# Kernel tuning notes

Hardware: AMD Instinct MI355X
Metric: run time of the kernel (lower is better)

## Reference

```python
import jax, jax.numpy as jnp
import numpy as np

N_EMBD = 1024
N_HEAD = 16
DIM_HEAD = N_EMBD // N_HEAD
# Source code divides scores by scale = dim_head**-0.5, i.e. multiplies by sqrt(dim_head).
INV_SCALE = 1.0 / (DIM_HEAD ** -0.5)


def setup_inputs() -> dict:
    key = jax.random.key(0)
    k1, k2, k3 = jax.random.split(key, 3)
    x = jax.random.normal(k1, (4, 2048, N_EMBD), dtype=jnp.float32)
    # Linear(n_embd, 3*n_embd, bias=False): y = x @ W_qkv  (W stored as [C, 3C])
    W_qkv = jax.random.normal(k2, (N_EMBD, 3 * N_EMBD), dtype=jnp.float32) * (N_EMBD ** -0.5)
    W_proj = jax.random.normal(k3, (N_EMBD, N_EMBD), dtype=jnp.float32) * (N_EMBD ** -0.5)
    return {"x": x, "W_qkv": W_qkv, "W_proj": W_proj}


def reference(x, W_qkv, W_proj):
    B, T, C = x.shape
    qkv = jnp.einsum('btc,cd->btd', x, W_qkv)  # [B,T,3C]
    q, k, v = jnp.split(qkv, 3, axis=-1)
    # [B,T,C] -> [B,H,T,Dh]
    def to_heads(t):
        return t.reshape(B, T, N_HEAD, DIM_HEAD).transpose(0, 2, 1, 3)
    q, k, v = to_heads(q), to_heads(k), to_heads(v)
    scores = jnp.einsum('bhqd,bhkd->bhqk', q, k) * INV_SCALE  # faithful to /scale bug
    causal = jnp.tril(jnp.ones((T, T), dtype=bool))
    scores = jnp.where(causal[None, None], scores, -jnp.inf)
    attn = jax.nn.softmax(scores, axis=-1)
    y = jnp.einsum('bhqk,bhkd->bhqd', attn, v)  # [B,H,T,Dh]
    y = y.transpose(0, 2, 1, 3).reshape(B, T, C)
    return jnp.einsum('btc,cd->btd', y, W_proj)
```

## Files before the change

### kernel.cpp

```cpp
#include <hip/hip_runtime.h>
#include <stdint.h>

typedef unsigned short ushort_t;
typedef __attribute__((ext_vector_type(8))) short short8;
typedef __attribute__((ext_vector_type(8))) _Float16 half8;
typedef __attribute__((ext_vector_type(4))) float f32x4;
typedef __attribute__((ext_vector_type(4))) unsigned short us4;

#define AS1 __attribute__((address_space(1)))
#define AS3 __attribute__((address_space(3)))

#if __has_builtin(__builtin_amdgcn_exp2f)
#define EXP2(x) __builtin_amdgcn_exp2f(x)
#else
#define EXP2(x) exp2f(x)
#endif

#define SC 11.541560327111707f

__device__ __forceinline__ ushort_t f2h(float f) {
  _Float16 h = (_Float16)f;
  return __builtin_bit_cast(unsigned short, h);
}

__device__ __forceinline__ void gload16(const void* g, void* l) {
  __builtin_amdgcn_global_load_lds((AS1 const void*)g, (AS3 void*)l, 16, 0, 0);
}

__device__ __forceinline__ f32x4 mfma16(short8 a, short8 b, f32x4 c) {
  return __builtin_amdgcn_mfma_f32_16x16x32_f16(
      __builtin_bit_cast(half8, a), __builtin_bit_cast(half8, b), c, 0, 0, 0);
}

__global__ __launch_bounds__(256) void cast_f32_f16(const float4* __restrict__ in,
                                                    us4* __restrict__ out, int n4) {
  int i = blockIdx.x * 256 + threadIdx.x;
  int stride = gridDim.x * 256;
  for (; i < n4; i += stride) {
    float4 v = in[i];
    us4 o;
    o[0] = f2h(v.x); o[1] = f2h(v.y); o[2] = f2h(v.z); o[3] = f2h(v.w);
    out[i] = o;
  }
}

__global__ __launch_bounds__(256) void tcast(const float* __restrict__ in,
                                             ushort_t* __restrict__ out, int R, int C) {
  __shared__ __align__(16) float lt[32][33];
  const int r0 = blockIdx.y * 32, c0 = blockIdx.x * 32;
  const int i = threadIdx.x;
  const int lr = i >> 3, lc = (i & 7) * 4;
  float4 v = *(const float4*)(in + (size_t)(r0 + lr) * C + c0 + lc);
  lt[lr][lc + 0] = v.x; lt[lr][lc + 1] = v.y; lt[lr][lc + 2] = v.z; lt[lr][lc + 3] = v.w;
  __syncthreads();
  const int oc = i >> 3;
  const int orr = (i & 7) * 4;
  us4 o;
#pragma unroll
  for (int jj = 0; jj < 4; ++jj) o[jj] = f2h(lt[orr + jj][oc]);
  *(us4*)(out + (size_t)(c0 + oc) * R + r0 + orr) = o;
}

template<int MODE>
__global__ __launch_bounds__(256) void gemm128(
    const ushort_t* __restrict__ A, const ushort_t* __restrict__ Bt, int K, int N,
    ushort_t* __restrict__ qo, ushort_t* __restrict__ ko, ushort_t* __restrict__ vo,
    float* __restrict__ outp)
{
  __shared__ __align__(16) unsigned char lds[32768];
  const int tid = threadIdx.x;
  const int lane = tid & 63, w = tid >> 6;
  const int ln = lane & 15, gq = lane >> 4;
  const int wr = w >> 1, wc = w & 1;
  const int m0 = blockIdx.y * 128, n0 = blockIdx.x * 128;
  const size_t ldb = (size_t)K * 2;
  const unsigned char* ab = (const unsigned char*)A + (size_t)m0 * ldb;
  const unsigned char* bb = (const unsigned char*)Bt + (size_t)n0 * ldb;
  f32x4 acc[4][4] = {};
  const int nkt = K >> 6;
  for (int kb = 0; kb < nkt; ++kb) {
    const unsigned char* abk = ab + kb * 128;
    const unsigned char* bbk = bb + kb * 128;
#pragma unroll
    for (int e = 0; e < 4; ++e) {
      unsigned o = e * 4096 + tid * 16;
      unsigned r = o >> 7;
      unsigned c = (o & 127) ^ ((r & 7) << 4);
      gload16(abk + (size_t)r * ldb + c, lds + o);
      gload16(bbk + (size_t)r * ldb + c, lds + 16384 + o);
    }
    __syncthreads();
    short8 af[4][2], bf8[4][2];
#pragma unroll
    for (int mi = 0; mi < 4; ++mi) {
      unsigned row = wr * 64 + mi * 16 + ln;
      unsigned c0 = (gq * 16) ^ ((row & 7) << 4);
      af[mi][0] = *(const short8*)(lds + row * 128 + c0);
      af[mi][1] = *(const short8*)(lds + row * 128 + (c0 ^ 64));
    }
#pragma unroll
    for (int ni = 0; ni < 4; ++ni) {
      unsigned row = wc * 64 + ni * 16 + ln;
      unsigned c0 = (gq * 16) ^ ((row & 7) << 4);
      bf8[ni][0] = *(const short8*)(lds + 16384 + row * 128 + c0);
      bf8[ni][1] = *(const short8*)(lds + 16384 + row * 128 + (c0 ^ 64));
    }
#pragma unroll
    for (int mi = 0; mi < 4; ++mi)
#pragma unroll
      for (int ni = 0; ni < 4; ++ni) {
        acc[mi][ni] = mfma16(af[mi][0], bf8[ni][0], acc[mi][ni]);
        acc[mi][ni] = mfma16(af[mi][1], bf8[ni][1], acc[mi][ni]);
      }
    __syncthreads();
  }
  if (MODE == 0) {
#pragma unroll
    for (int mi = 0; mi < 4; ++mi)
#pragma unroll
      for (int ni = 0; ni < 4; ++ni) {
        int feat = n0 + wc * 64 + ni * 16 + ln;
        int sec = feat >> 10, cc = feat & 1023;
        int hh = cc >> 6, dd = cc & 63;
        int tokbase = m0 + wr * 64 + mi * 16 + gq * 4;
        int bh = (tokbase >> 11) * 16 + hh;
        int tloc = tokbase & 2047;
        if (sec == 2) {
          us4 pk;
#pragma unroll
          for (int j = 0; j < 4; ++j) pk[j] = f2h(acc[mi][ni][j]);
          *(us4*)(vo + ((size_t)bh * 64 + dd) * 2048 + tloc) = pk;
        } else {
          ushort_t* dst = (sec == 0) ? qo : ko;
#pragma unroll
          for (int j = 0; j < 4; ++j) {
            size_t off = ((size_t)bh * 2048 + tloc + j) * 64 + dd;
            dst[off] = f2h(acc[mi][ni][j]);
          }
        }
      }
  } else {
#pragma unroll
    for (int mi = 0; mi < 4; ++mi)
#pragma unroll
      for (int ni = 0; ni < 4; ++ni)
#pragma unroll
        for (int j = 0; j < 4; ++j) {
          int token = m0 + wr * 64 + mi * 16 + gq * 4 + j;
          int feat  = n0 + wc * 64 + ni * 16 + ln;
          outp[(size_t)token * N + feat] = acc[mi][ni][j];
        }
  }
}

__global__ __launch_bounds__(256) void attn_kernel(const ushort_t* __restrict__ qg,
                                                   const ushort_t* __restrict__ kg,
                                                   const ushort_t* __restrict__ vtg,
                                                   ushort_t* __restrict__ yg) {
  __shared__ __align__(16) unsigned char lds[40960];
  const int n = blockIdx.x;
  const int xcd = n & 7, loc = n >> 3;
  const int bh = xcd * 8 + (loc >> 4);
  const int pair = loc & 15;
  const int tid = threadIdx.x;
  const int lane = tid & 63, w = tid >> 6;
  const int ln = lane & 15, gq = lane >> 4;

  const unsigned char* kbase = (const unsigned char*)kg + (size_t)bh * 2048 * 128;
  const unsigned char* vbase = (const unsigned char*)vtg + (size_t)bh * 64 * 4096;
  const ushort_t* qg_bh = qg + (size_t)bh * 2048 * 64;
  const unsigned pw = 32768 + w * 2048;

  auto stage = [&](int buf, int t) {
    const unsigned char* kt = kbase + (size_t)t * 8192;
    const unsigned char* vt = vbase + t * 128;
#pragma unroll
    for (int e = 0; e < 2; ++e) {
      unsigned o = e * 4096 + tid * 16;
      unsigned r = o >> 7;
      unsigned c = (o & 127) ^ ((r & 7) << 4);
      gload16(kt + r * 128 + c, lds + buf * 8192 + o);
      gload16(vt + (size_t)r * 4096 + c, lds + 16384 + buf * 8192 + o);
    }
  };

  int cur = 0;
  for (int ph = 0; ph < 2; ++ph) {
    const int qt = (ph == 0) ? pair : 31 - pair;
    const int q0 = qt * 64;
    const int nt = qt + 1;

    const ushort_t* qrow = qg_bh + (size_t)(q0 + w * 16 + ln) * 64;
    short8 qa0 = *(const short8*)(qrow + gq * 8);
    short8 qa1 = *(const short8*)(qrow + 32 + gq * 8);

    f32x4 yacc[4] = {};
    float mrow = -3e38f, lrow = 0.f;

    stage(cur, 0);
    __syncthreads();

    for (int t = 0; t < nt; ++t) {
      if (t + 1 < nt) stage(cur ^ 1, t + 1);
      const unsigned kb_ = cur * 8192;
      const unsigned vb_ = 16384 + cur * 8192;
      f32x4 s[4];
      __builtin_amdgcn_s_setprio(1);
#pragma unroll
      for (int f = 0; f < 4; ++f) {
        unsigned row = f * 16 + ln;
        unsigned c0 = (gq * 16) ^ ((row & 7) << 4);
        short8 k0 = *(const short8*)(lds + kb_ + row * 128 + c0);
        short8 k1 = *(const short8*)(lds + kb_ + row * 128 + (c0 ^ 64));
        f32x4 z = {0.f, 0.f, 0.f, 0.f};
        z = mfma16(k0, qa0, z);
        s[f] = mfma16(k1, qa1, z);
      }
      __builtin_amdgcn_s_setprio(0);
      if (t == nt - 1) {
        int qloc = w * 16 + ln;
#pragma unroll
        for (int f = 0; f < 4; ++f) {
          int kvb = f * 16 + gq * 4;
#pragma unroll
          for (int j = 0; j < 4; ++j)
            if (kvb + j > qloc) s[f][j] = -3e38f;
        }
      }
      {
        float rm = s[0][0];
#pragma unroll
        for (int f = 0; f < 4; ++f)
#pragma unroll
          for (int j = 0; j < 4; ++j) rm = fmaxf(rm, s[f][j]);
        rm = fmaxf(rm, __shfl_xor(rm, 16));
        rm = fmaxf(rm, __shfl_xor(rm, 32));
        if (__any((rm - mrow) * SC > 8.0f)) {
          float mnew = fmaxf(mrow, rm);
          float alpha = EXP2((mrow - mnew) * SC);
          lrow *= alpha;
          mrow = mnew;
#pragma unroll
          for (int j = 0; j < 4; ++j) {
            float aj = __shfl(alpha, gq * 4 + j);
#pragma unroll
            for (int df = 0; df < 4; ++df) yacc[df][j] *= aj;
          }
        }
        float msc = mrow * SC;
        float rs = 0.f;
#pragma unroll
        for (int f = 0; f < 4; ++f)
#pragma unroll
          for (int j = 0; j < 4; ++j) {
            float p = EXP2(__builtin_fmaf(s[f][j], SC, -msc));
            s[f][j] = p;
            rs += p;
          }
        rs += __shfl_xor(rs, 16);
        rs += __shfl_xor(rs, 32);
        lrow += rs;
      }
#pragma unroll
      for (int f = 0; f < 4; ++f) {
        us4 pk;
#pragma unroll
        for (int j = 0; j < 4; ++j) pk[j] = f2h(s[f][j]);
        unsigned addr = (pw + ln * 128 + (f * 16 + gq * 4) * 2) ^ ((ln & 7) << 4);
        *(us4*)(lds + addr) = pk;
      }
      __builtin_amdgcn_s_setprio(1);
#pragma unroll
      for (int st = 0; st < 2; ++st) {
        unsigned pc = (st * 64 + gq * 16) ^ ((ln & 7) << 4);
        short8 pa = *(const short8*)(lds + pw + ln * 128 + pc);
#pragma unroll
        for (int df = 0; df < 4; ++df) {
          unsigned row = df * 16 + ln;
          unsigned c0 = (st * 64 + gq * 16) ^ ((row & 7) << 4);
          short8 vb = *(const short8*)(lds + vb_ + row * 128 + c0);
          yacc[df] = mfma16(pa, vb, yacc[df]);
        }
      }
      __builtin_amdgcn_s_setprio(0);
      __syncthreads();
      cur ^= 1;
    }

#pragma unroll
    for (int j = 0; j < 4; ++j) {
      float lj = __shfl(lrow, gq * 4 + j);
      float rl = 1.0f / lj;
      int tq = q0 + w * 16 + gq * 4 + j;
#pragma unroll
      for (int df = 0; df < 4; ++df) {
        int col = (bh & 15) * 64 + df * 16 + ln;
        size_t off = ((size_t)(bh >> 4) * 2048 + tq) * 1024 + col;
        yg[off] = f2h(yacc[df][j] * rl);
      }
    }
  }
}

extern "C" void kernel_launch(void* const* d_in, const int* in_sizes, int n_in,
                              void* d_out, int out_size, void* d_ws, size_t ws_size,
                              hipStream_t stream) {
  (void)in_sizes; (void)n_in; (void)out_size; (void)ws_size;
  const float* x     = (const float*)d_in[0];
  const float* wqkv  = (const float*)d_in[1];
  const float* wproj = (const float*)d_in[2];
  float* out = (float*)d_out;
  char* ws = (char*)d_ws;
  ushort_t* xb   = (ushort_t*)(ws);
  ushort_t* wqkt = (ushort_t*)(ws + 16777216);
  ushort_t* wpt  = (ushort_t*)(ws + 23068672);
  ushort_t* qb_  = (ushort_t*)(ws + 25165824);
  ushort_t* kb_  = (ushort_t*)(ws + 41943040);
  ushort_t* vt   = (ushort_t*)(ws + 75497472);
  ushort_t* yb   = xb;

  cast_f32_f16<<<2048, 256, 0, stream>>>((const float4*)x, (us4*)xb, 2097152);
  tcast<<<dim3(96, 32), 256, 0, stream>>>(wqkv, wqkt, 1024, 3072);
  tcast<<<dim3(32, 32), 256, 0, stream>>>(wproj, wpt, 1024, 1024);
  gemm128<0><<<dim3(24, 64), 256, 0, stream>>>(xb, wqkt, 1024, 3072, qb_, kb_, vt, nullptr);
  attn_kernel<<<1024, 256, 0, stream>>>(qb_, kb_, vt, yb);
  gemm128<1><<<dim3(8, 64), 256, 0, stream>>>(yb, wpt, 1024, 1024, nullptr, nullptr, nullptr, out);
}
```

Before: 186.7 us.

## Load K and V fragments directly from global memory instead of LDS staging

Removes the double-buffered asynchronous LDS staging of K and V tiles and the per-iteration block barrier. Each wave now reads its K and V^T MFMA fragments straight from global memory into registers, and LDS shrinks to the per-wave P scratch. This cuts LDS footprint and synchronization, which may raise occupancy. The cost is that all four waves load the same K/V data redundantly through L1/L2 and global latency is no longer hidden by prefetch.

```diff
diff --git a/kernel.cpp b/kernel.cpp
--- a/kernel.cpp
+++ b/kernel.cpp
@@ -157,7 +157,7 @@
                                                    const ushort_t* __restrict__ kg,
                                                    const ushort_t* __restrict__ vtg,
                                                    ushort_t* __restrict__ yg) {
-  __shared__ __align__(16) unsigned char lds[40960];
+  __shared__ __align__(16) unsigned char lds[8192];
   const int n = blockIdx.x;
   const int xcd = n & 7, loc = n >> 3;
   const int bh = xcd * 8 + (loc >> 4);
@@ -166,25 +166,11 @@
   const int lane = tid & 63, w = tid >> 6;
   const int ln = lane & 15, gq = lane >> 4;
 
-  const unsigned char* kbase = (const unsigned char*)kg + (size_t)bh * 2048 * 128;
-  const unsigned char* vbase = (const unsigned char*)vtg + (size_t)bh * 64 * 4096;
+  const ushort_t* kg_bh = kg + (size_t)bh * 2048 * 64;
+  const ushort_t* vt_bh = vtg + (size_t)bh * 64 * 2048;
   const ushort_t* qg_bh = qg + (size_t)bh * 2048 * 64;
-  const unsigned pw = 32768 + w * 2048;
-
-  auto stage = [&](int buf, int t) {
-    const unsigned char* kt = kbase + (size_t)t * 8192;
-    const unsigned char* vt = vbase + t * 128;
-#pragma unroll
-    for (int e = 0; e < 2; ++e) {
-      unsigned o = e * 4096 + tid * 16;
-      unsigned r = o >> 7;
-      unsigned c = (o & 127) ^ ((r & 7) << 4);
-      gload16(kt + r * 128 + c, lds + buf * 8192 + o);
-      gload16(vt + (size_t)r * 4096 + c, lds + 16384 + buf * 8192 + o);
-    }
-  };
-
-  int cur = 0;
+  const unsigned pw = w * 2048;
+
   for (int ph = 0; ph < 2; ++ph) {
     const int qt = (ph == 0) ? pair : 31 - pair;
     const int q0 = qt * 64;
@@ -197,24 +183,22 @@
     f32x4 yacc[4] = {};
     float mrow = -3e38f, lrow = 0.f;
 
-    stage(cur, 0);
-    __syncthreads();
-
     for (int t = 0; t < nt; ++t) {
-      if (t + 1 < nt) stage(cur ^ 1, t + 1);
-      const unsigned kb_ = cur * 8192;
-      const unsigned vb_ = 16384 + cur * 8192;
+      const ushort_t* kt_g = kg_bh + (size_t)t * 64 * 64;
+      short8 kf0[4], kf1[4];
+#pragma unroll
+      for (int f = 0; f < 4; ++f) {
+        const ushort_t* kr = kt_g + (unsigned)(f * 16 + ln) * 64 + gq * 8;
+        kf0[f] = *(const short8*)kr;
+        kf1[f] = *(const short8*)(kr + 32);
+      }
       f32x4 s[4];
       __builtin_amdgcn_s_setprio(1);
 #pragma unroll
       for (int f = 0; f < 4; ++f) {
-        unsigned row = f * 16 + ln;
-        unsigned c0 = (gq * 16) ^ ((row & 7) << 4);
-        short8 k0 = *(const short8*)(lds + kb_ + row * 128 + c0);
-        short8 k1 = *(const short8*)(lds + kb_ + row * 128 + (c0 ^ 64));
         f32x4 z = {0.f, 0.f, 0.f, 0.f};
-        z = mfma16(k0, qa0, z);
-        s[f] = mfma16(k1, qa1, z);
+        z = mfma16(kf0[f], qa0, z);
+        s[f] = mfma16(kf1[f], qa1, z);
       }
       __builtin_amdgcn_s_setprio(0);
       if (t == nt - 1) {
@@ -269,6 +253,7 @@
         unsigned addr = (pw + ln * 128 + (f * 16 + gq * 4) * 2) ^ ((ln & 7) << 4);
         *(us4*)(lds + addr) = pk;
       }
+      const ushort_t* vt_t = vt_bh + t * 64;
       __builtin_amdgcn_s_setprio(1);
 #pragma unroll
       for (int st = 0; st < 2; ++st) {
@@ -276,15 +261,12 @@
         short8 pa = *(const short8*)(lds + pw + ln * 128 + pc);
 #pragma unroll
         for (int df = 0; df < 4; ++df) {
-          unsigned row = df * 16 + ln;
-          unsigned c0 = (st * 64 + gq * 16) ^ ((row & 7) << 4);
-          short8 vb = *(const short8*)(lds + vb_ + row * 128 + c0);
+          const ushort_t* vr = vt_t + (size_t)(df * 16 + ln) * 2048 + st * 32 + gq * 8;
+          short8 vb = *(const short8*)vr;
           yacc[df] = mfma16(pa, vb, yacc[df]);
         }
       }
       __builtin_amdgcn_s_setprio(0);
-      __syncthreads();
-      cur ^= 1;
     }
 
 #pragma unroll
```

Measured after the change: 395.6 us. +111.9%, slower.

## Split attention into one q-tile per block with 32-wide KV tiles

Applied to the files above, without the earlier changes.

The attention kernel now launches one block per 64-row query tile instead of pairing two tiles per block, doubling the grid and ordering tiles longest-first. KV tiles shrink from 64 to 32 keys, which halves LDS use and adds a launch-bounds occupancy hint so more blocks can share a CU. The cost is twice as many loop iterations and barriers per query tile, smaller MFMA batches per iteration, and the V/P LDS layouts losing their XOR swizzle, which may cause bank conflicts.

```diff
diff --git a/kernel.cpp b/kernel.cpp
--- a/kernel.cpp
+++ b/kernel.cpp
@@ -153,15 +153,16 @@
   }
 }
 
-__global__ __launch_bounds__(256) void attn_kernel(const ushort_t* __restrict__ qg,
-                                                   const ushort_t* __restrict__ kg,
-                                                   const ushort_t* __restrict__ vtg,
-                                                   ushort_t* __restrict__ yg) {
-  __shared__ __align__(16) unsigned char lds[40960];
+__global__ __launch_bounds__(256, 8) void attn_kernel(const ushort_t* __restrict__ qg,
+                                                      const ushort_t* __restrict__ kg,
+                                                      const ushort_t* __restrict__ vtg,
+                                                      ushort_t* __restrict__ yg) {
+  __shared__ __align__(16) unsigned char lds[20480];
   const int n = blockIdx.x;
   const int xcd = n & 7, loc = n >> 3;
-  const int bh = xcd * 8 + (loc >> 4);
-  const int pair = loc & 15;
+  const int bh = xcd * 8 + (loc >> 5);
+  const int qi = loc & 31;
+  const int qt = (qi & 1) ? (qi >> 1) : 31 - (qi >> 1);
   const int tid = threadIdx.x;
   const int lane = tid & 63, w = tid >> 6;
   const int ln = lane & 15, gq = lane >> 4;
@@ -169,135 +170,131 @@
   const unsigned char* kbase = (const unsigned char*)kg + (size_t)bh * 2048 * 128;
   const unsigned char* vbase = (const unsigned char*)vtg + (size_t)bh * 64 * 4096;
   const ushort_t* qg_bh = qg + (size_t)bh * 2048 * 64;
-  const unsigned pw = 32768 + w * 2048;
+  const unsigned pw = 16384 + w * 1024;
+
+  const int q0 = qt * 64;
+  const int nt2 = 2 * qt + 2;
 
   auto stage = [&](int buf, int t) {
-    const unsigned char* kt = kbase + (size_t)t * 8192;
-    const unsigned char* vt = vbase + t * 128;
-#pragma unroll
-    for (int e = 0; e < 2; ++e) {
-      unsigned o = e * 4096 + tid * 16;
+    const unsigned char* kt = kbase + (size_t)t * 4096;
+    const unsigned char* vt = vbase + t * 64;
+    unsigned o = tid * 16;
+    {
       unsigned r = o >> 7;
       unsigned c = (o & 127) ^ ((r & 7) << 4);
-      gload16(kt + r * 128 + c, lds + buf * 8192 + o);
-      gload16(vt + (size_t)r * 4096 + c, lds + 16384 + buf * 8192 + o);
+      gload16(kt + r * 128 + c, lds + buf * 4096 + o);
+    }
+    {
+      unsigned r = o >> 6;
+      unsigned c = o & 63;
+      gload16(vt + (size_t)r * 4096 + c, lds + 8192 + buf * 4096 + o);
     }
   };
 
+  const ushort_t* qrow = qg_bh + (size_t)(q0 + w * 16 + ln) * 64;
+  short8 qa0 = *(const short8*)(qrow + gq * 8);
+  short8 qa1 = *(const short8*)(qrow + 32 + gq * 8);
+
+  f32x4 yacc[4] = {};
+  float mrow = -3e38f, lrow = 0.f;
+  const int qglob = q0 + w * 16 + ln;
+
   int cur = 0;
-  for (int ph = 0; ph < 2; ++ph) {
-    const int qt = (ph == 0) ? pair : 31 - pair;
-    const int q0 = qt * 64;
-    const int nt = qt + 1;
-
-    const ushort_t* qrow = qg_bh + (size_t)(q0 + w * 16 + ln) * 64;
-    short8 qa0 = *(const short8*)(qrow + gq * 8);
-    short8 qa1 = *(const short8*)(qrow + 32 + gq * 8);
-
-    f32x4 yacc[4] = {};
-    float mrow = -3e38f, lrow = 0.f;
-
-    stage(cur, 0);
+  stage(cur, 0);
+  __syncthreads();
+
+  for (int t = 0; t < nt2; ++t) {
+    if (t + 1 < nt2) stage(cur ^ 1, t + 1);
+    const unsigned kb_ = cur * 4096;
+    const unsigned vb_ = 8192 + cur * 4096;
+    f32x4 s[2];
+    __builtin_amdgcn_s_setprio(1);
+#pragma unroll
+    for (int f = 0; f < 2; ++f) {
+      unsigned row = f * 16 + ln;
+      unsigned c0 = (gq * 16) ^ ((row & 7) << 4);
+      short8 k0 = *(const short8*)(lds + kb_ + row * 128 + c0);
+      short8 k1 = *(const short8*)(lds + kb_ + row * 128 + (c0 ^ 64));
+      f32x4 z = {0.f, 0.f, 0.f, 0.f};
+      z = mfma16(k0, qa0, z);
+      s[f] = mfma16(k1, qa1, z);
+    }
+    __builtin_amdgcn_s_setprio(0);
+    if (t >= nt2 - 2) {
+      const int kv0 = t * 32;
+#pragma unroll
+      for (int f = 0; f < 2; ++f) {
+        int kvb = kv0 + f * 16 + gq * 4;
+#pragma unroll
+        for (int j = 0; j < 4; ++j)
+          if (kvb + j > qglob) s[f][j] = -3e38f;
+      }
+    }
+    {
+      float rm = s[0][0];
+#pragma unroll
+      for (int f = 0; f < 2; ++f)
+#pragma unroll
+        for (int j = 0; j < 4; ++j) rm = fmaxf(rm, s[f][j]);
+      rm = fmaxf(rm, __shfl_xor(rm, 16));
+      rm = fmaxf(rm, __shfl_xor(rm, 32));
+      if (__any((rm - mrow) * SC > 8.0f)) {
+        float mnew = fmaxf(mrow, rm);
+        float alpha = EXP2((mrow - mnew) * SC);
+        lrow *= alpha;
+        mrow = mnew;
+#pragma unroll
+        for (int j = 0; j < 4; ++j) {
+          float aj = __shfl(alpha, gq * 4 + j);
+#pragma unroll
+          for (int df = 0; df < 4; ++df) yacc[df][j] *= aj;
+        }
+      }
+      float msc = mrow * SC;
+      float rs = 0.f;
+#pragma unroll
+      for (int f = 0; f < 2; ++f)
+#pragma unroll
+        for (int j = 0; j < 4; ++j) {
+          float p = EXP2(__builtin_fmaf(s[f][j], SC, -msc));
+          s[f][j] = p;
+          rs += p;
+        }
+      rs += __shfl_xor(rs, 16);
+      rs += __shfl_xor(rs, 32);
+      lrow += rs;
+    }
+#pragma unroll
+    for (int f = 0; f < 2; ++f) {
+      us4 pk;
+#pragma unroll
+      for (int j = 0; j < 4; ++j) pk[j] = f2h(s[f][j]);
+      *(us4*)(lds + pw + ln * 64 + f * 32 + gq * 8) = pk;
+    }
+    __builtin_amdgcn_s_setprio(1);
+    {
+      short8 pa = *(const short8*)(lds + pw + ln * 64 + gq * 16);
+#pragma unroll
+      for (int df = 0; df < 4; ++df) {
+        short8 vb = *(const short8*)(lds + vb_ + (df * 16 + ln) * 64 + gq * 16);
+        yacc[df] = mfma16(pa, vb, yacc[df]);
+      }
+    }
+    __builtin_amdgcn_s_setprio(0);
     __syncthreads();
-
-    for (int t = 0; t < nt; ++t) {
-      if (t + 1 < nt) stage(cur ^ 1, t + 1);
-      const unsigned kb_ = cur * 8192;
-      const unsigned vb_ = 16384 + cur * 8192;
-      f32x4 s[4];
-      __builtin_amdgcn_s_setprio(1);
-#pragma unroll
-      for (int f = 0; f < 4; ++f) {
-        unsigned row = f * 16 + ln;
-        unsigned c0 = (gq * 16) ^ ((row & 7) << 4);
-        short8 k0 = *(const short8*)(lds + kb_ + row * 128 + c0);
-        short8 k1 = *(const short8*)(lds + kb_ + row * 128 + (c0 ^ 64));
-        f32x4 z = {0.f, 0.f, 0.f, 0.f};
-        z = mfma16(k0, qa0, z);
-        s[f] = mfma16(k1, qa1, z);
-      }
-      __builtin_amdgcn_s_setprio(0);
-      if (t == nt - 1) {
-        int qloc = w * 16 + ln;
-#pragma unroll
-        for (int f = 0; f < 4; ++f) {
-          int kvb = f * 16 + gq * 4;
-#pragma unroll
-          for (int j = 0; j < 4; ++j)
-            if (kvb + j > qloc) s[f][j] = -3e38f;
-        }
-      }
-      {
-        float rm = s[0][0];
-#pragma unroll
-        for (int f = 0; f < 4; ++f)
-#pragma unroll
-          for (int j = 0; j < 4; ++j) rm = fmaxf(rm, s[f][j]);
-        rm = fmaxf(rm, __shfl_xor(rm, 16));
-        rm = fmaxf(rm, __shfl_xor(rm, 32));
-        if (__any((rm - mrow) * SC > 8.0f)) {
-          float mnew = fmaxf(mrow, rm);
-          float alpha = EXP2((mrow - mnew) * SC);
-          lrow *= alpha;
-          mrow = mnew;
-#pragma unroll
-          for (int j = 0; j < 4; ++j) {
-            float aj = __shfl(alpha, gq * 4 + j);
-#pragma unroll
-            for (int df = 0; df < 4; ++df) yacc[df][j] *= aj;
-          }
-        }
-        float msc = mrow * SC;
-        float rs = 0.f;
-#pragma unroll
-        for (int f = 0; f < 4; ++f)
-#pragma unroll
-          for (int j = 0; j < 4; ++j) {
-            float p = EXP2(__builtin_fmaf(s[f][j], SC, -msc));
-            s[f][j] = p;
-            rs += p;
-          }
-        rs += __shfl_xor(rs, 16);
-        rs += __shfl_xor(rs, 32);
-        lrow += rs;
-      }
-#pragma unroll
-      for (int f = 0; f < 4; ++f) {
-        us4 pk;
-#pragma unroll
-        for (int j = 0; j < 4; ++j) pk[j] = f2h(s[f][j]);
-        unsigned addr = (pw + ln * 128 + (f * 16 + gq * 4) * 2) ^ ((ln & 7) << 4);
-        *(us4*)(lds + addr) = pk;
-      }
-      __builtin_amdgcn_s_setprio(1);
-#pragma unroll
-      for (int st = 0; st < 2; ++st) {
-        unsigned pc = (st * 64 + gq * 16) ^ ((ln & 7) << 4);
-        short8 pa = *(const short8*)(lds + pw + ln * 128 + pc);
-#pragma unroll
-        for (int df = 0; df < 4; ++df) {
-          unsigned row = df * 16 + ln;
-          unsigned c0 = (st * 64 + gq * 16) ^ ((row & 7) << 4);
-          short8 vb = *(const short8*)(lds + vb_ + row * 128 + c0);
-          yacc[df] = mfma16(pa, vb, yacc[df]);
-        }
-      }
-      __builtin_amdgcn_s_setprio(0);
-      __syncthreads();
-      cur ^= 1;
-    }
-
-#pragma unroll
-    for (int j = 0; j < 4; ++j) {
-      float lj = __shfl(lrow, gq * 4 + j);
-      float rl = 1.0f / lj;
-      int tq = q0 + w * 16 + gq * 4 + j;
-#pragma unroll
-      for (int df = 0; df < 4; ++df) {
-        int col = (bh & 15) * 64 + df * 16 + ln;
-        size_t off = ((size_t)(bh >> 4) * 2048 + tq) * 1024 + col;
-        yg[off] = f2h(yacc[df][j] * rl);
-      }
+    cur ^= 1;
+  }
+
+#pragma unroll
+  for (int j = 0; j < 4; ++j) {
+    float lj = __shfl(lrow, gq * 4 + j);
+    float rl = 1.0f / lj;
+    int tq = q0 + w * 16 + gq * 4 + j;
+#pragma unroll
+    for (int df = 0; df < 4; ++df) {
+      int col = (bh & 15) * 64 + df * 16 + ln;
+      size_t off = ((size_t)(bh >> 4) * 2048 + tq) * 1024 + col;
+      yg[off] = f2h(yacc[df][j] * rl);
     }
   }
 }
@@ -323,6 +320,6 @@
   tcast<<<dim3(96, 32), 256, 0, stream>>>(wqkv, wqkt, 1024, 3072);
   tcast<<<dim3(32, 32), 256, 0, stream>>>(wproj, wpt, 1024, 1024);
   gemm128<0><<<dim3(24, 64), 256, 0, stream>>>(xb, wqkt, 1024, 3072, qb_, kb_, vt, nullptr);
-  attn_kernel<<<1024, 256, 0, stream>>>(qb_, kb_, vt, yb);
+  attn_kernel<<<2048, 256, 0, stream>>>(qb_, kb_, vt, yb);
   gemm128<1><<<dim3(8, 64), 256, 0, stream>>>(yb, wpt, 1024, 1024, nullptr, nullptr, nullptr, out);
 }
```

Result: slower. 274.7 us (+47.2%).

## Process both paired causal query tiles in one K/V sweep

Applied to the files above, without the earlier changes.

The attention kernel previously handled its two paired query tiles (qt and 31-qt) in two separate passes, each streaming its own K/V tiles. Now both tiles' Q fragments are held in registers and a single pass over K/V tiles feeds both, with tile A active only up to its causal limit. This removes the redundant reload of K/V tiles shared by both queries, and the pair index is also permuted to vary work order across blocks. In exchange, register pressure roughly doubles for accumulators and softmax state, which may reduce occupancy, and the P staging buffer in LDS is reused back-to-back without a barrier between the A and B stages.

```diff
diff --git a/kernel.cpp b/kernel.cpp
--- a/kernel.cpp
+++ b/kernel.cpp
@@ -161,7 +161,11 @@
   const int n = blockIdx.x;
   const int xcd = n & 7, loc = n >> 3;
   const int bh = xcd * 8 + (loc >> 4);
-  const int pair = loc & 15;
+  const int pr = loc & 15;
+  const int pair = (pr & 1) ? (pr >> 1) : 15 - (pr >> 1);
+  const int qA = pair, qB = 31 - pair;
+  const int q0A = qA * 64, q0B = qB * 64;
+  const int nt = qB + 1;
   const int tid = threadIdx.x;
   const int lane = tid & 63, w = tid >> 6;
   const int ln = lane & 15, gq = lane >> 4;
@@ -184,88 +188,96 @@
     }
   };
 
+  const ushort_t* qrowA = qg_bh + (size_t)(q0A + w * 16 + ln) * 64;
+  const ushort_t* qrowB = qg_bh + (size_t)(q0B + w * 16 + ln) * 64;
+  short8 qaA0 = *(const short8*)(qrowA + gq * 8);
+  short8 qaA1 = *(const short8*)(qrowA + 32 + gq * 8);
+  short8 qaB0 = *(const short8*)(qrowB + gq * 8);
+  short8 qaB1 = *(const short8*)(qrowB + 32 + gq * 8);
+
+  f32x4 yaccA[4] = {}, yaccB[4] = {};
+  float mrowA = -3e38f, lrowA = 0.f;
+  float mrowB = -3e38f, lrowB = 0.f;
+
   int cur = 0;
-  for (int ph = 0; ph < 2; ++ph) {
-    const int qt = (ph == 0) ? pair : 31 - pair;
-    const int q0 = qt * 64;
-    const int nt = qt + 1;
-
-    const ushort_t* qrow = qg_bh + (size_t)(q0 + w * 16 + ln) * 64;
-    short8 qa0 = *(const short8*)(qrow + gq * 8);
-    short8 qa1 = *(const short8*)(qrow + 32 + gq * 8);
-
-    f32x4 yacc[4] = {};
-    float mrow = -3e38f, lrow = 0.f;
-
-    stage(cur, 0);
-    __syncthreads();
-
-    for (int t = 0; t < nt; ++t) {
-      if (t + 1 < nt) stage(cur ^ 1, t + 1);
-      const unsigned kb_ = cur * 8192;
-      const unsigned vb_ = 16384 + cur * 8192;
-      f32x4 s[4];
-      __builtin_amdgcn_s_setprio(1);
-#pragma unroll
-      for (int f = 0; f < 4; ++f) {
-        unsigned row = f * 16 + ln;
-        unsigned c0 = (gq * 16) ^ ((row & 7) << 4);
-        short8 k0 = *(const short8*)(lds + kb_ + row * 128 + c0);
-        short8 k1 = *(const short8*)(lds + kb_ + row * 128 + (c0 ^ 64));
-        f32x4 z = {0.f, 0.f, 0.f, 0.f};
-        z = mfma16(k0, qa0, z);
-        s[f] = mfma16(k1, qa1, z);
-      }
-      __builtin_amdgcn_s_setprio(0);
-      if (t == nt - 1) {
+  stage(cur, 0);
+  __syncthreads();
+
+  for (int t = 0; t < nt; ++t) {
+    if (t + 1 < nt) stage(cur ^ 1, t + 1);
+    const unsigned kb_ = cur * 8192;
+    const unsigned vb_ = 16384 + cur * 8192;
+    const bool doA = (t <= qA);
+
+    f32x4 sA[4], sB[4];
+    __builtin_amdgcn_s_setprio(1);
+#pragma unroll
+    for (int f = 0; f < 4; ++f) {
+      unsigned row = f * 16 + ln;
+      unsigned c0 = (gq * 16) ^ ((row & 7) << 4);
+      short8 k0 = *(const short8*)(lds + kb_ + row * 128 + c0);
+      short8 k1 = *(const short8*)(lds + kb_ + row * 128 + (c0 ^ 64));
+      f32x4 zB = {0.f, 0.f, 0.f, 0.f};
+      zB = mfma16(k0, qaB0, zB);
+      sB[f] = mfma16(k1, qaB1, zB);
+      if (doA) {
+        f32x4 zA = {0.f, 0.f, 0.f, 0.f};
+        zA = mfma16(k0, qaA0, zA);
+        sA[f] = mfma16(k1, qaA1, zA);
+      }
+    }
+    __builtin_amdgcn_s_setprio(0);
+
+    if (doA) {
+      if (t == qA) {
         int qloc = w * 16 + ln;
 #pragma unroll
         for (int f = 0; f < 4; ++f) {
           int kvb = f * 16 + gq * 4;
 #pragma unroll
           for (int j = 0; j < 4; ++j)
-            if (kvb + j > qloc) s[f][j] = -3e38f;
+            if (kvb + j > qloc) sA[f][j] = -3e38f;
         }
       }
       {
-        float rm = s[0][0];
+        float rm = sA[0][0];
 #pragma unroll
         for (int f = 0; f < 4; ++f)
 #pragma unroll
-          for (int j = 0; j < 4; ++j) rm = fmaxf(rm, s[f][j]);
+          for (int j = 0; j < 4; ++j) rm = fmaxf(rm, sA[f][j]);
         rm = fmaxf(rm, __shfl_xor(rm, 16));
         rm = fmaxf(rm, __shfl_xor(rm, 32));
-        if (__any((rm - mrow) * SC > 8.0f)) {
-          float mnew = fmaxf(mrow, rm);
-          float alpha = EXP2((mrow - mnew) * SC);
-          lrow *= alpha;
-          mrow = mnew;
+        if (__any((rm - mrowA) * SC > 8.0f)) {
+          float mnew = fmaxf(mrowA, rm);
+          float alpha = EXP2((mrowA - mnew) * SC);
+          lrowA *= alpha;
+          mrowA = mnew;
 #pragma unroll
           for (int j = 0; j < 4; ++j) {
             float aj = __shfl(alpha, gq * 4 + j);
 #pragma unroll
-            for (int df = 0; df < 4; ++df) yacc[df][j] *= aj;
+            for (int df = 0; df < 4; ++df) yaccA[df][j] *= aj;
           }
         }
-        float msc = mrow * SC;
+        float msc = mrowA * SC;
         float rs = 0.f;
 #pragma unroll
         for (int f = 0; f < 4; ++f)
 #pragma unroll
           for (int j = 0; j < 4; ++j) {
-            float p = EXP2(__builtin_fmaf(s[f][j], SC, -msc));
-            s[f][j] = p;
+            float p = EXP2(__builtin_fmaf(sA[f][j], SC, -msc));
+            sA[f][j] = p;
             rs += p;
           }
         rs += __shfl_xor(rs, 16);
         rs += __shfl_xor(rs, 32);
-        lrow += rs;
+        lrowA += rs;
       }
 #pragma unroll
       for (int f = 0; f < 4; ++f) {
         us4 pk;
 #pragma unroll
-        for (int j = 0; j < 4; ++j) pk[j] = f2h(s[f][j]);
+        for (int j = 0; j < 4; ++j) pk[j] = f2h(sA[f][j]);
         unsigned addr = (pw + ln * 128 + (f * 16 + gq * 4) * 2) ^ ((ln & 7) << 4);
         *(us4*)(lds + addr) = pk;
       }
@@ -279,25 +291,98 @@
           unsigned row = df * 16 + ln;
           unsigned c0 = (st * 64 + gq * 16) ^ ((row & 7) << 4);
           short8 vb = *(const short8*)(lds + vb_ + row * 128 + c0);
-          yacc[df] = mfma16(pa, vb, yacc[df]);
+          yaccA[df] = mfma16(pa, vb, yaccA[df]);
         }
       }
       __builtin_amdgcn_s_setprio(0);
-      __syncthreads();
-      cur ^= 1;
-    }
-
-#pragma unroll
-    for (int j = 0; j < 4; ++j) {
-      float lj = __shfl(lrow, gq * 4 + j);
-      float rl = 1.0f / lj;
-      int tq = q0 + w * 16 + gq * 4 + j;
-#pragma unroll
-      for (int df = 0; df < 4; ++df) {
-        int col = (bh & 15) * 64 + df * 16 + ln;
-        size_t off = ((size_t)(bh >> 4) * 2048 + tq) * 1024 + col;
-        yg[off] = f2h(yacc[df][j] * rl);
-      }
+    }
+
+    {
+      if (t == qB) {
+        int qloc = w * 16 + ln;
+#pragma unroll
+        for (int f = 0; f < 4; ++f) {
+          int kvb = f * 16 + gq * 4;
+#pragma unroll
+          for (int j = 0; j < 4; ++j)
+            if (kvb + j > qloc) sB[f][j] = -3e38f;
+        }
+      }
+      {
+        float rm = sB[0][0];
+#pragma unroll
+        for (int f = 0; f < 4; ++f)
+#pragma unroll
+          for (int j = 0; j < 4; ++j) rm = fmaxf(rm, sB[f][j]);
+        rm = fmaxf(rm, __shfl_xor(rm, 16));
+        rm = fmaxf(rm, __shfl_xor(rm, 32));
+        if (__any((rm - mrowB) * SC > 8.0f)) {
+          float mnew = fmaxf(mrowB, rm);
+          float alpha = EXP2((mrowB - mnew) * SC);
+          lrowB *= alpha;
+          mrowB = mnew;
+#pragma unroll
+          for (int j = 0; j < 4; ++j) {
+            float aj = __shfl(alpha, gq * 4 + j);
+#pragma unroll
+            for (int df = 0; df < 4; ++df) yaccB[df][j] *= aj;
+          }
+        }
+        float msc = mrowB * SC;
+        float rs = 0.f;
+#pragma unroll
+        for (int f = 0; f < 4; ++f)
+#pragma unroll
+          for (int j = 0; j < 4; ++j) {
+            float p = EXP2(__builtin_fmaf(sB[f][j], SC, -msc));
+            sB[f][j] = p;
+            rs += p;
+          }
+        rs += __shfl_xor(rs, 16);
+        rs += __shfl_xor(rs, 32);
+        lrowB += rs;
+      }
+#pragma unroll
+      for (int f = 0; f < 4; ++f) {
+        us4 pk;
+#pragma unroll
+        for (int j = 0; j < 4; ++j) pk[j] = f2h(sB[f][j]);
+        unsigned addr = (pw + ln * 128 + (f * 16 + gq * 4) * 2) ^ ((ln & 7) << 4);
+        *(us4*)(lds + addr) = pk;
+      }
+      __builtin_amdgcn_s_setprio(1);
+#pragma unroll
+      for (int st = 0; st < 2; ++st) {
+        unsigned pc = (st * 64 + gq * 16) ^ ((ln & 7) << 4);
+        short8 pa = *(const short8*)(lds + pw + ln * 128 + pc);
+#pragma unroll
+        for (int df = 0; df < 4; ++df) {
+          unsigned row = df * 16 + ln;
+          unsigned c0 = (st * 64 + gq * 16) ^ ((row & 7) << 4);
+          short8 vb = *(const short8*)(lds + vb_ + row * 128 + c0);
+          yaccB[df] = mfma16(pa, vb, yaccB[df]);
+        }
+      }
+      __builtin_amdgcn_s_setprio(0);
+    }
+
+    __syncthreads();
+    cur ^= 1;
+  }
+
+#pragma unroll
+  for (int j = 0; j < 4; ++j) {
+    float ljA = __shfl(lrowA, gq * 4 + j);
+    float ljB = __shfl(lrowB, gq * 4 + j);
+    float rlA = 1.0f / ljA;
+    float rlB = 1.0f / ljB;
+    int tqA = q0A + w * 16 + gq * 4 + j;
+    int tqB = q0B + w * 16 + gq * 4 + j;
+#pragma unroll
+    for (int df = 0; df < 4; ++df) {
+      int col = (bh & 15) * 64 + df * 16 + ln;
+      yg[((size_t)(bh >> 4) * 2048 + tqA) * 1024 + col] = f2h(yaccA[df][j] * rlA);
+      yg[((size_t)(bh >> 4) * 2048 + tqB) * 1024 + col] = f2h(yaccB[df][j] * rlB);
     }
   }
 }
```

After: 200.0 us. +7.1%, slower.
